# Kernel tuning notes

Measured on AMD Instinct MI355X. Metric: run time of the kernel, lower is better.

Reference implementation:

```python
import jax, jax.numpy as jnp
import numpy as np

R = 32  # reduced channel dim = outplane // reduction
TRI_I, TRI_J = np.triu_indices(R)  # static upper-triangle indices (528 pairs)


def setup_inputs() -> dict:
    key = jax.random.key(0)
    k1, k2, k3 = jax.random.split(key, 3)
    B, Cin, H, W = 8, 256, 96, 96
    Cout = 256
    tri = R * (R + 1) // 2  # 528
    x = jax.random.normal(k1, (B, Cin, H, W), dtype=jnp.float32)
    # 1x1 conv weights stored as [out, in] matrices
    w_reduce = jax.random.normal(k2, (R, Cin), dtype=jnp.float32) * (1.0 / np.sqrt(Cin))
    w_recover = jax.random.normal(k3, (Cout, tri), dtype=jnp.float32) * (1.0 / np.sqrt(tri))
    return {"x": x, "w_reduce": w_reduce, "w_recover": w_recover}


def reference(x, w_reduce, w_recover):
    # reduce: 1x1 conv (no bias): [B,Cin,H,W] -> [B,R,H,W]
    out = jnp.einsum('bchw,rc->brhw', x, w_reduce)
    # per-pixel outer product, but only the upper-triangle entries:
    # bilinear[b,i,j,h,w] = out[b,i,h,w] * out[b,j,h,w]; gather (i,j) in triu
    i = jnp.asarray(TRI_I)
    j = jnp.asarray(TRI_J)
    up = out[:, i, :, :] * out[:, j, :, :]  # [B, 528, H, W]
    # channelRecover: 1x1 conv 528 -> Cout
    y = jnp.einsum('bthw,ot->bohw', up, w_recover)
    # signed sqrt
    return jnp.sign(y) * jnp.sqrt(jnp.abs(y) + 1e-6)
```

## Files before the change

kernel.cpp:

```cpp
#include <hip/hip_runtime.h>
#include <hip/hip_bf16.h>
#include <math.h>

#define HW     9216
#define CIN    256
#define RCH    32
#define NTRI   528
#define COUT   256
#define NB     8
#define W16ROW 544
#define UPROW  296

typedef _Float16 f16x8 __attribute__((ext_vector_type(8)));
typedef _Float16 f16x4 __attribute__((ext_vector_type(4)));
typedef float    f32x4 __attribute__((ext_vector_type(4)));

struct TriTab { unsigned char i[544]; unsigned char j[544]; };
constexpr TriTab make_tri() {
  TriTab t{};
  int ii = 0, jj = 0;
  for (int k = 0; k < 544; ++k) {
    if (k < NTRI) {
      t.i[k] = (unsigned char)ii; t.j[k] = (unsigned char)jj;
      if (++jj == 32) { ++ii; jj = ii; }
    } else { t.i[k] = 0; t.j[k] = 0; }
  }
  return t;
}
constexpr TriTab TRI = make_tri();

template<int TQ, int HALF>
__device__ __forceinline__ void build_up(const float (&o)[RCH], _Float16* rowp) {
  constexpr int NG  = HALF ? 8 : 9;
  constexpr int TLB = TQ * (HALF ? 32 : 36);
  constexpr int TB  = HALF ? 288 : 0;
#pragma unroll
  for (int g = 0; g < NG; ++g) {
    f16x4 v;
#pragma unroll
    for (int s = 0; s < 4; ++s) {
      const int tl = TLB + g * 4 + s;
      const int t  = TB + tl;
      float f = (t < NTRI) ? o[TRI.i[t]] * o[TRI.j[t]] : 0.0f;
      v[s] = (_Float16)f;
    }
    *(f16x4*)&rowp[TLB + g * 4] = v;
  }
}

template<int HALF>
__device__ __forceinline__ void build_dispatch(int wv, const float (&o)[RCH],
                                               _Float16* rowp) {
  switch (wv) {
    case 0: build_up<0, HALF>(o, rowp); break;
    case 1: build_up<1, HALF>(o, rowp); break;
    case 2: build_up<2, HALF>(o, rowp); break;
    case 3: build_up<3, HALF>(o, rowp); break;
    case 4: build_up<4, HALF>(o, rowp); break;
    case 5: build_up<5, HALF>(o, rowp); break;
    case 6: build_up<6, HALF>(o, rowp); break;
    default: build_up<7, HALF>(o, rowp); break;
  }
}

__global__ __launch_bounds__(256) void convert_kernel(
    const float* __restrict__ w_reduce, const float* __restrict__ w_recover,
    _Float16* __restrict__ w16, _Float16* __restrict__ wr16h,
    _Float16* __restrict__ wr16l) {
  const int bx = blockIdx.x;
  const int tid = threadIdx.x;
  if (bx < COUT) {
    for (int t = tid; t < W16ROW; t += 256) {
      float f = (t < NTRI) ? w_recover[(size_t)bx * NTRI + t] : 0.0f;
      w16[(size_t)bx * W16ROW + t] = (_Float16)f;
    }
  } else {
    int e = (bx - COUT) * 512 + tid;
#pragma unroll
    for (int k = 0; k < 2; ++k, e += 256) {
      float f = w_reduce[e];
      _Float16 h = (_Float16)f;
      wr16h[e] = h;
      wr16l[e] = (_Float16)(f - (float)h);
    }
  }
}

__global__ __launch_bounds__(512, 4) void fused_kernel(
    const float* __restrict__ x, const _Float16* __restrict__ w16,
    const _Float16* __restrict__ wr16h, const _Float16* __restrict__ wr16l,
    float* __restrict__ y) {
  __shared__ float outS[RCH * 68];
  __shared__ __align__(16) _Float16 upS[64 * UPROW];

  const int tid  = threadIdx.x;
  const int bx   = blockIdx.x;
  const int b    = bx / 144;
  const int p0   = (bx - b * 144) * 64;
  const int wv   = tid >> 6;
  const int lane = tid & 63;
  const int ml   = lane & 15;
  const int q    = lane >> 4;
  const int mt   = wv >> 2;
  const int nt   = wv & 3;

  {
    f32x4 g1acc;
#pragma unroll
    for (int r2 = 0; r2 < 4; ++r2) g1acc[r2] = 0.0f;

    const float* xb = x + (size_t)b * CIN * HW + p0 + nt * 16 + ml;
#pragma unroll
    for (int ch = 0; ch < 8; ++ch) {
      const int c0 = ch * 32;
      float xv[8];
#pragma unroll
      for (int s = 0; s < 8; ++s)
        xv[s] = xb[(size_t)(c0 + q * 8 + s) * HW];
      f16x8 bh, bl;
#pragma unroll
      for (int s = 0; s < 8; ++s) {
        _Float16 h = (_Float16)xv[s];
        bh[s] = h;
        bl[s] = (_Float16)(xv[s] - (float)h);
      }
      const int off = (mt * 16 + ml) * CIN + c0 + q * 8;
      f16x8 ah = *(const f16x8*)&wr16h[off];
      f16x8 al = *(const f16x8*)&wr16l[off];
      g1acc = __builtin_amdgcn_mfma_f32_16x16x32_f16(ah, bh, g1acc, 0, 0, 0);
      g1acc = __builtin_amdgcn_mfma_f32_16x16x32_f16(al, bh, g1acc, 0, 0, 0);
      g1acc = __builtin_amdgcn_mfma_f32_16x16x32_f16(ah, bl, g1acc, 0, 0, 0);
    }
#pragma unroll
    for (int reg = 0; reg < 4; ++reg)
      outS[(mt * 16 + q * 4 + reg) * 68 + nt * 16 + ml] = g1acc[reg];
  }
  __syncthreads();

  f32x4 acc[2][4];
#pragma unroll
  for (int mi = 0; mi < 2; ++mi)
#pragma unroll
    for (int ni = 0; ni < 4; ++ni)
#pragma unroll
      for (int r2 = 0; r2 < 4; ++r2) acc[mi][ni][r2] = 0.0f;

  _Float16* rowp = &upS[lane * UPROW];

  {
    float o[RCH];
#pragma unroll
    for (int r = 0; r < RCH; ++r) o[r] = outS[r * 68 + lane];
    build_dispatch<0>(wv, o, rowp);
  }
  __syncthreads();
#pragma unroll
  for (int c = 0; c < 9; ++c) {
    const int t0 = c * 32;
    f16x8 afr[2];
#pragma unroll
    for (int mi = 0; mi < 2; ++mi)
      afr[mi] = *(const f16x8*)&w16[(size_t)(wv * 32 + mi * 16 + ml) * W16ROW + t0 + q * 8];
    f16x8 bfr[4];
#pragma unroll
    for (int ni = 0; ni < 4; ++ni)
      bfr[ni] = *(const f16x8*)&upS[(ni * 16 + ml) * UPROW + t0 + q * 8];
#pragma unroll
    for (int mi = 0; mi < 2; ++mi)
#pragma unroll
      for (int ni = 0; ni < 4; ++ni)
        acc[mi][ni] = __builtin_amdgcn_mfma_f32_16x16x32_f16(afr[mi], bfr[ni], acc[mi][ni], 0, 0, 0);
  }
  __syncthreads();

  {
    float o[RCH];
#pragma unroll
    for (int r = 0; r < RCH; ++r) o[r] = outS[r * 68 + lane];
    build_dispatch<1>(wv, o, rowp);
  }
  __syncthreads();
#pragma unroll
  for (int c = 0; c < 8; ++c) {
    const int t0l = c * 32;
    const int t0g = 288 + c * 32;
    f16x8 afr[2];
#pragma unroll
    for (int mi = 0; mi < 2; ++mi)
      afr[mi] = *(const f16x8*)&w16[(size_t)(wv * 32 + mi * 16 + ml) * W16ROW + t0g + q * 8];
    f16x8 bfr[4];
#pragma unroll
    for (int ni = 0; ni < 4; ++ni)
      bfr[ni] = *(const f16x8*)&upS[(ni * 16 + ml) * UPROW + t0l + q * 8];
#pragma unroll
    for (int mi = 0; mi < 2; ++mi)
#pragma unroll
      for (int ni = 0; ni < 4; ++ni)
        acc[mi][ni] = __builtin_amdgcn_mfma_f32_16x16x32_f16(afr[mi], bfr[ni], acc[mi][ni], 0, 0, 0);
  }

#pragma unroll
  for (int mi = 0; mi < 2; ++mi) {
#pragma unroll
    for (int reg = 0; reg < 4; ++reg) {
      const int o = wv * 32 + mi * 16 + q * 4 + reg;
      float* yrow = y + ((size_t)(b * COUT + o)) * HW + p0 + ml;
#pragma unroll
      for (int ni = 0; ni < 4; ++ni) {
        float v = acc[mi][ni][reg];
        float s = sqrtf(fabsf(v) + 1e-6f);
        yrow[ni * 16] = v > 0.0f ? s : (v < 0.0f ? -s : 0.0f);
      }
    }
  }
}

extern "C" void kernel_launch(void* const* d_in, const int* in_sizes, int n_in,
                              void* d_out, int out_size, void* d_ws, size_t ws_size,
                              hipStream_t stream) {
  const float* x         = (const float*)d_in[0];
  const float* w_reduce  = (const float*)d_in[1];
  const float* w_recover = (const float*)d_in[2];
  float* y = (float*)d_out;

  _Float16* w16   = (_Float16*)d_ws;
  _Float16* wr16h = (_Float16*)((char*)d_ws + 278528);
  _Float16* wr16l = (_Float16*)((char*)d_ws + 278528 + 16384);

  convert_kernel<<<COUT + 16, 256, 0, stream>>>(w_reduce, w_recover, w16, wr16h, wr16l);
  fused_kernel<<<NB * (HW / 64), 512, 0, stream>>>(x, w16, wr16h, wr16l, y);
}
```

Baseline: 187.5 us.

## Pre-swizzle recover weights into fragment order and double-buffer MFMA operand loads

```diff
diff --git a/kernel.cpp b/kernel.cpp
--- a/kernel.cpp
+++ b/kernel.cpp
@@ -8,7 +8,7 @@
 #define NTRI   528
 #define COUT   256
 #define NB     8
-#define W16ROW 544
+#define WFROWS 272
 #define UPROW  296
 
 typedef _Float16 f16x8 __attribute__((ext_vector_type(8)));
@@ -69,13 +69,22 @@
     _Float16* __restrict__ wr16l) {
   const int bx = blockIdx.x;
   const int tid = threadIdx.x;
-  if (bx < COUT) {
-    for (int t = tid; t < W16ROW; t += 256) {
-      float f = (t < NTRI) ? w_recover[(size_t)bx * NTRI + t] : 0.0f;
-      w16[(size_t)bx * W16ROW + t] = (_Float16)f;
-    }
+  if (bx < WFROWS) {
+    const int wv  = bx / 34;
+    const int rem = bx - wv * 34;
+    const int mi  = rem / 17;
+    const int c   = rem - mi * 17;
+    const int lane = tid >> 2;
+    const int s0   = (tid & 3) * 2;
+    const int o = wv * 32 + mi * 16 + (lane & 15);
+    const int t = c * 32 + (lane >> 4) * 8 + s0;
+    float f0 = (t     < NTRI) ? w_recover[(size_t)o * NTRI + t]     : 0.0f;
+    float f1 = (t + 1 < NTRI) ? w_recover[(size_t)o * NTRI + t + 1] : 0.0f;
+    _Float16* p = &w16[((size_t)bx * 64 + lane) * 8 + s0];
+    p[0] = (_Float16)f0;
+    p[1] = (_Float16)f1;
   } else {
-    int e = (bx - COUT) * 512 + tid;
+    int e = (bx - WFROWS) * 512 + tid;
 #pragma unroll
     for (int k = 0; k < 2; ++k, e += 256) {
       float f = w_reduce[e];
@@ -110,21 +119,24 @@
     for (int r2 = 0; r2 < 4; ++r2) g1acc[r2] = 0.0f;
 
     const float* xb = x + (size_t)b * CIN * HW + p0 + nt * 16 + ml;
+    float xv[64];
+#pragma unroll
+    for (int ch = 0; ch < 8; ++ch)
+#pragma unroll
+      for (int s = 0; s < 8; ++s)
+        xv[ch * 8 + s] = xb[(size_t)(ch * 32 + q * 8 + s) * HW];
+
 #pragma unroll
     for (int ch = 0; ch < 8; ++ch) {
-      const int c0 = ch * 32;
-      float xv[8];
-#pragma unroll
-      for (int s = 0; s < 8; ++s)
-        xv[s] = xb[(size_t)(c0 + q * 8 + s) * HW];
       f16x8 bh, bl;
 #pragma unroll
       for (int s = 0; s < 8; ++s) {
-        _Float16 h = (_Float16)xv[s];
+        float f = xv[ch * 8 + s];
+        _Float16 h = (_Float16)f;
         bh[s] = h;
-        bl[s] = (_Float16)(xv[s] - (float)h);
+        bl[s] = (_Float16)(f - (float)h);
       }
-      const int off = (mt * 16 + ml) * CIN + c0 + q * 8;
+      const int off = (mt * 16 + ml) * CIN + ch * 32 + q * 8;
       f16x8 ah = *(const f16x8*)&wr16h[off];
       f16x8 al = *(const f16x8*)&wr16l[off];
       g1acc = __builtin_amdgcn_mfma_f32_16x16x32_f16(ah, bh, g1acc, 0, 0, 0);
@@ -135,6 +147,14 @@
     for (int reg = 0; reg < 4; ++reg)
       outS[(mt * 16 + q * 4 + reg) * 68 + nt * 16 + ml] = g1acc[reg];
   }
+
+  const _Float16* wf0 = w16 + ((size_t)(wv * 2 + 0) * 17 * 64 + lane) * 8;
+  const _Float16* wf1 = w16 + ((size_t)(wv * 2 + 1) * 17 * 64 + lane) * 8;
+
+  f16x8 abuf[2][2];
+  abuf[0][0] = *(const f16x8*)&wf0[0];
+  abuf[0][1] = *(const f16x8*)&wf1[0];
+
   __syncthreads();
 
   f32x4 acc[2][4];
@@ -154,22 +174,28 @@
     build_dispatch<0>(wv, o, rowp);
   }
   __syncthreads();
+
+  f16x8 bbuf[2][4];
+#pragma unroll
+  for (int ni = 0; ni < 4; ++ni)
+    bbuf[0][ni] = *(const f16x8*)&upS[(ni * 16 + ml) * UPROW + q * 8];
+
 #pragma unroll
   for (int c = 0; c < 9; ++c) {
-    const int t0 = c * 32;
-    f16x8 afr[2];
-#pragma unroll
-    for (int mi = 0; mi < 2; ++mi)
-      afr[mi] = *(const f16x8*)&w16[(size_t)(wv * 32 + mi * 16 + ml) * W16ROW + t0 + q * 8];
-    f16x8 bfr[4];
-#pragma unroll
-    for (int ni = 0; ni < 4; ++ni)
-      bfr[ni] = *(const f16x8*)&upS[(ni * 16 + ml) * UPROW + t0 + q * 8];
-#pragma unroll
-    for (int mi = 0; mi < 2; ++mi)
+    const int cur = c & 1, nxt = cur ^ 1;
+    abuf[nxt][0] = *(const f16x8*)&wf0[(size_t)(c + 1) * 512];
+    abuf[nxt][1] = *(const f16x8*)&wf1[(size_t)(c + 1) * 512];
+    if (c < 8) {
+      const int t0n = (c + 1) * 32;
 #pragma unroll
       for (int ni = 0; ni < 4; ++ni)
-        acc[mi][ni] = __builtin_amdgcn_mfma_f32_16x16x32_f16(afr[mi], bfr[ni], acc[mi][ni], 0, 0, 0);
+        bbuf[nxt][ni] = *(const f16x8*)&upS[(ni * 16 + ml) * UPROW + t0n + q * 8];
+    }
+#pragma unroll
+    for (int ni = 0; ni < 4; ++ni) {
+      acc[0][ni] = __builtin_amdgcn_mfma_f32_16x16x32_f16(abuf[cur][0], bbuf[cur][ni], acc[0][ni], 0, 0, 0);
+      acc[1][ni] = __builtin_amdgcn_mfma_f32_16x16x32_f16(abuf[cur][1], bbuf[cur][ni], acc[1][ni], 0, 0, 0);
+    }
   }
   __syncthreads();
 
@@ -180,23 +206,28 @@
     build_dispatch<1>(wv, o, rowp);
   }
   __syncthreads();
-#pragma unroll
-  for (int c = 0; c < 8; ++c) {
-    const int t0l = c * 32;
-    const int t0g = 288 + c * 32;
-    f16x8 afr[2];
-#pragma unroll
-    for (int mi = 0; mi < 2; ++mi)
-      afr[mi] = *(const f16x8*)&w16[(size_t)(wv * 32 + mi * 16 + ml) * W16ROW + t0g + q * 8];
-    f16x8 bfr[4];
-#pragma unroll
-    for (int ni = 0; ni < 4; ++ni)
-      bfr[ni] = *(const f16x8*)&upS[(ni * 16 + ml) * UPROW + t0l + q * 8];
-#pragma unroll
-    for (int mi = 0; mi < 2; ++mi)
+
+#pragma unroll
+  for (int ni = 0; ni < 4; ++ni)
+    bbuf[0][ni] = *(const f16x8*)&upS[(ni * 16 + ml) * UPROW + q * 8];
+
+#pragma unroll
+  for (int cc = 0; cc < 8; ++cc) {
+    const int ca = (cc + 1) & 1;
+    const int cb = cc & 1, nb = cb ^ 1;
+    if (cc < 7) {
+      abuf[ca ^ 1][0] = *(const f16x8*)&wf0[(size_t)(10 + cc) * 512];
+      abuf[ca ^ 1][1] = *(const f16x8*)&wf1[(size_t)(10 + cc) * 512];
+      const int t0n = (cc + 1) * 32;
 #pragma unroll
       for (int ni = 0; ni < 4; ++ni)
-        acc[mi][ni] = __builtin_amdgcn_mfma_f32_16x16x32_f16(afr[mi], bfr[ni], acc[mi][ni], 0, 0, 0);
+        bbuf[nb][ni] = *(const f16x8*)&upS[(ni * 16 + ml) * UPROW + t0n + q * 8];
+    }
+#pragma unroll
+    for (int ni = 0; ni < 4; ++ni) {
+      acc[0][ni] = __builtin_amdgcn_mfma_f32_16x16x32_f16(abuf[ca][0], bbuf[cb][ni], acc[0][ni], 0, 0, 0);
+      acc[1][ni] = __builtin_amdgcn_mfma_f32_16x16x32_f16(abuf[ca][1], bbuf[cb][ni], acc[1][ni], 0, 0, 0);
+    }
   }
 
 #pragma unroll
@@ -227,6 +258,6 @@
   _Float16* wr16h = (_Float16*)((char*)d_ws + 278528);
   _Float16* wr16l = (_Float16*)((char*)d_ws + 278528 + 16384);
 
-  convert_kernel<<<COUT + 16, 256, 0, stream>>>(w_reduce, w_recover, w16, wr16h, wr16l);
+  convert_kernel<<<WFROWS + 16, 256, 0, stream>>>(w_reduce, w_recover, w16, wr16h, wr16l);
   fused_kernel<<<NB * (HW / 64), 512, 0, stream>>>(x, w16, wr16h, wr16l, y);
 }
```

New measurement: 176.6 us. -5.8%, faster.
